# Kernel optimization log

Hardware: AMD Instinct MI355X
Metric: run time of the kernel (lower is better)

Reference implementation:

```python
import math
import jax, jax.numpy as jnp
import numpy as np

B, T, D, H = 4, 1024, 1024, 8
HD = D // H  # head_dim = 128

def _trigram_dirs():
    # 8 trigrams = all sign combinations in {−1,+1}^3, L2-normalized (p=2, dim=1)
    t = np.array([[(i >> b & 1) * 2 - 1 for b in (2, 1, 0)] for i in range(8)], dtype=np.float32)
    return jnp.asarray(t / np.linalg.norm(t, axis=1, keepdims=True))

def setup_inputs() -> dict:
    key = jax.random.key(0)
    k1, k2, k3, k4 = jax.random.split(key, 4)
    x = jax.random.normal(k1, (B, T, D), dtype=jnp.float32)
    Wqkv = jax.random.normal(k2, (D, 3 * D), dtype=jnp.float32) * 0.02
    Wout = jax.random.normal(k3, (D, D), dtype=jnp.float32) * 0.02
    # head_scales init to 0 in the module; use nonzero values so the geo-bias path is exercised
    head_scales = jax.random.normal(k4, (H,), dtype=jnp.float32) * 0.1
    head_dirs = _trigram_dirs()  # [H, 3] buffer
    return {"x": x, "Wqkv": Wqkv, "Wout": Wout, "head_scales": head_scales, "head_dirs": head_dirs}

def reference(x, Wqkv, Wout, head_scales, head_dirs):
    b, t, d = x.shape
    scale = 1.0 / math.sqrt(HD)
    qkv = (x @ Wqkv).reshape(b, t, 3, H, HD)
    qkv = jnp.transpose(qkv, (2, 0, 3, 1, 4))  # [3, B, H, T, HD]
    q, k, v = qkv[0], qkv[1], qkv[2]
    # scores: [B, H, T, T]
    scores = jnp.einsum('bhqd,bhkd->bhqk', q, k) * scale
    # rank-1 trigram geometric bias from first 3 dims of q/k
    q_proj = jnp.einsum('bhtd,hd->bht', q[..., :3], head_dirs)
    k_proj = jnp.einsum('bhtd,hd->bht', k[..., :3], head_dirs)
    geo_bias = q_proj[..., :, None] * k_proj[..., None, :]  # [B, H, T, T]
    scores = scores + head_scales[None, :, None, None] * geo_bias
    causal = jnp.tril(jnp.ones((t, t), dtype=bool))
    scores = jnp.where(causal, scores, -jnp.inf)
    attn = jax.nn.softmax(scores, axis=-1)
    out = jnp.einsum('bhqk,bhkd->bhqd', attn, v)  # [B, H, T, HD]
    out = jnp.transpose(out, (0, 2, 1, 3)).reshape(b, t, d)
    return out @ Wout
```

## Files before the change

kernel.cpp:

```cpp
#include <hip/hip_runtime.h>
#include <stdint.h>

typedef __attribute__((ext_vector_type(8))) short short8;
typedef __attribute__((ext_vector_type(4))) short short4v;
typedef __attribute__((ext_vector_type(4))) float f32x4;

__device__ __forceinline__ short f2bf(float x) {
  union { float f; uint32_t u; } c; c.f = x;
  uint32_t r = (c.u + 0x7FFFu + ((c.u >> 16) & 1u)) >> 16;
  return (short)r;
}
__device__ __forceinline__ float b2f(short s) {
  union { uint32_t u; float f; } c; c.u = ((uint32_t)(uint16_t)s) << 16;
  return c.f;
}
__device__ __forceinline__ uint32_t pack2bf(float lo, float hi) {
  return ((uint32_t)(uint16_t)f2bf(hi) << 16) | (uint32_t)(uint16_t)f2bf(lo);
}

__global__ __launch_bounds__(256) void prep_kernel(const float* __restrict__ x,
                                                   const float* __restrict__ Wqkv,
                                                   const float* __restrict__ Wout,
                                                   short* __restrict__ xb,
                                                   short* __restrict__ wqkvT,
                                                   short* __restrict__ woutT) {
  __shared__ __align__(16) short tile[32][33];
  const int bid = blockIdx.x;
  if (bid < 2048) {
    const int n4 = (4 * 1024 * 1024) / 4;
    int i = bid * 256 + threadIdx.x;
    for (; i < n4; i += 2048 * 256) {
      float4 v = reinterpret_cast<const float4*>(x)[i];
      short4v o;
      o.x = f2bf(v.x); o.y = f2bf(v.y); o.z = f2bf(v.z); o.w = f2bf(v.w);
      reinterpret_cast<short4v*>(xb)[i] = o;
    }
  } else {
    const float* in;
    short* out;
    int K, N, bx, by;
    if (bid < 2048 + 3072) {
      const int idx = bid - 2048;
      in = Wqkv; out = wqkvT; K = 1024; N = 3072; bx = idx % 96; by = idx / 96;
    } else {
      const int idx = bid - 5120;
      in = Wout; out = woutT; K = 1024; N = 1024; bx = idx % 32; by = idx / 32;
    }
    const int nb = bx * 32, kb = by * 32;
    const int tx = threadIdx.x & 31, ty = threadIdx.x >> 5;
#pragma unroll
    for (int i = 0; i < 32; i += 8)
      tile[ty + i][tx] = f2bf(in[(size_t)(kb + ty + i) * N + nb + tx]);
    __syncthreads();
#pragma unroll
    for (int i = 0; i < 32; i += 8)
      out[(size_t)(nb + ty + i) * K + kb + tx] = tile[tx][ty + i];
  }
}

__global__ __launch_bounds__(256) void vtrans_kernel(const short* __restrict__ qkvb,
                                                     short* __restrict__ vT) {
  __shared__ __align__(16) short tile[64][65];
  const int bid = blockIdx.x;
  const int b = bid / 256;
  const int kv0 = (bid % 16) * 64, c0 = ((bid / 16) % 16) * 64;
  const int tx = threadIdx.x & 15, ty = threadIdx.x >> 4;
  const short* src = qkvb + (size_t)(b * 1024) * 3072 + 2048;
#pragma unroll
  for (int i = 0; i < 64; i += 16) {
    int r = ty + i;
#pragma unroll
    for (int j = 0; j < 4; ++j)
      tile[r][tx * 4 + j] = src[(size_t)(kv0 + r) * 3072 + c0 + tx * 4 + j];
  }
  __syncthreads();
  short* dst = vT + (size_t)b * 1024 * 1024;
#pragma unroll
  for (int i = 0; i < 64; i += 16) {
    int cc = ty + i;
#pragma unroll
    for (int j = 0; j < 4; ++j)
      dst[(size_t)(c0 + cc) * 1024 + kv0 + tx * 4 + j] = tile[tx * 4 + j][cc];
  }
}

template <int OUT_BF16>
__global__ __launch_bounds__(256) void gemm_kernel(const short* __restrict__ A,
                                                   const short* __restrict__ Bt,
                                                   void* __restrict__ Cout,
                                                   int K, int ldc) {
  __shared__ __align__(16) short Al[2][128 * 32];
  __shared__ __align__(16) short Bl[2][128 * 32];
  const int t = threadIdx.x;
  const int lane = t & 63, w = t >> 6;
  const int wr = w >> 1, wc = w & 1;
  const int g = lane >> 4, c16 = lane & 15;
  const int row0 = blockIdx.y * 128, col0 = blockIdx.x * 128;

  f32x4 acc[4][4];
#pragma unroll
  for (int m = 0; m < 4; ++m)
#pragma unroll
    for (int n = 0; n < 4; ++n) {
      f32x4 z = {0.0f, 0.0f, 0.0f, 0.0f};
      acc[m][n] = z;
    }

  auto stage = [&](int buf, int kt) {
    const int k0 = kt * 32;
#pragma unroll
    for (int i = 0; i < 2; ++i) {
      const int qb = i * 256 + (t & 192);
      const int q = qb + lane;
      const int r = q >> 2;
      const int c = (q & 3) ^ ((r >> 1) & 3);
      const short* ga = A + (size_t)(row0 + r) * K + k0 + c * 8;
      const short* gb = Bt + (size_t)(col0 + r) * K + k0 + c * 8;
      __builtin_amdgcn_global_load_lds((const __attribute__((address_space(1))) void*)ga,
                                       (__attribute__((address_space(3))) void*)&Al[buf][qb * 8],
                                       16, 0, 0);
      __builtin_amdgcn_global_load_lds((const __attribute__((address_space(1))) void*)gb,
                                       (__attribute__((address_space(3))) void*)&Bl[buf][qb * 8],
                                       16, 0, 0);
    }
  };

  stage(0, 0);
  __syncthreads();
  const int NK = K >> 5;
  int cur = 0;
  const int rA0 = wr * 64 + c16;
  const int rB0 = wc * 64 + c16;
  for (int kt = 0; kt < NK; ++kt) {
    if (kt + 1 < NK) stage(cur ^ 1, kt + 1);
    short8 aF[4], bF[4];
#pragma unroll
    for (int m = 0; m < 4; ++m) {
      const int r = rA0 + m * 16;
      const int c = g ^ ((r >> 1) & 3);
      aF[m] = *reinterpret_cast<const short8*>(&Al[cur][r * 32 + c * 8]);
    }
#pragma unroll
    for (int n = 0; n < 4; ++n) {
      const int r = rB0 + n * 16;
      const int c = g ^ ((r >> 1) & 3);
      bF[n] = *reinterpret_cast<const short8*>(&Bl[cur][r * 32 + c * 8]);
    }
#pragma unroll
    for (int m = 0; m < 4; ++m)
#pragma unroll
      for (int n = 0; n < 4; ++n)
        acc[m][n] = __builtin_amdgcn_mfma_f32_16x16x32_bf16(aF[m], bF[n], acc[m][n], 0, 0, 0);
    __syncthreads();
    cur ^= 1;
  }

  const int er = row0 + wr * 64 + g * 4;
  const int ec = col0 + wc * 64 + c16;
#pragma unroll
  for (int m = 0; m < 4; ++m)
#pragma unroll
    for (int n = 0; n < 4; ++n)
#pragma unroll
      for (int j = 0; j < 4; ++j) {
        const size_t off = (size_t)(er + m * 16 + j) * ldc + ec + n * 16;
        if (OUT_BF16)
          ((short*)Cout)[off] = f2bf(acc[m][n][j]);
        else
          ((float*)Cout)[off] = acc[m][n][j];
      }
}

template <int OUT_BF16>
__global__ __launch_bounds__(256) void gemm64_kernel(const short* __restrict__ A,
                                                     const short* __restrict__ Bt,
                                                     void* __restrict__ Cout,
                                                     int K, int ldc) {
  __shared__ __align__(16) short Al[2][128 * 32];
  __shared__ __align__(16) short Bl[2][64 * 32];
  const int t = threadIdx.x;
  const int lane = t & 63, w = t >> 6;
  const int wr = w >> 1, wc = w & 1;
  const int g = lane >> 4, c16 = lane & 15;
  const int row0 = blockIdx.y * 128, col0 = blockIdx.x * 64;

  f32x4 acc[4][2];
#pragma unroll
  for (int m = 0; m < 4; ++m)
#pragma unroll
    for (int n = 0; n < 2; ++n) {
      f32x4 z = {0.0f, 0.0f, 0.0f, 0.0f};
      acc[m][n] = z;
    }

  auto stage = [&](int buf, int kt) {
    const int k0 = kt * 32;
#pragma unroll
    for (int i = 0; i < 2; ++i) {
      const int qb = i * 256 + (t & 192);
      const int q = qb + lane;
      const int r = q >> 2;
      const int c = (q & 3) ^ ((r >> 1) & 3);
      const short* ga = A + (size_t)(row0 + r) * K + k0 + c * 8;
      __builtin_amdgcn_global_load_lds((const __attribute__((address_space(1))) void*)ga,
                                       (__attribute__((address_space(3))) void*)&Al[buf][qb * 8],
                                       16, 0, 0);
    }
    {
      const int qb = (t & 192);
      const int q = qb + lane;
      const int r = q >> 2;
      const int c = (q & 3) ^ ((r >> 1) & 3);
      const short* gb = Bt + (size_t)(col0 + r) * K + k0 + c * 8;
      __builtin_amdgcn_global_load_lds((const __attribute__((address_space(1))) void*)gb,
                                       (__attribute__((address_space(3))) void*)&Bl[buf][qb * 8],
                                       16, 0, 0);
    }
  };

  stage(0, 0);
  __syncthreads();
  const int NK = K >> 5;
  int cur = 0;
  const int rA0 = wr * 64 + c16;
  const int rB0 = wc * 32 + c16;
  for (int kt = 0; kt < NK; ++kt) {
    if (kt + 1 < NK) stage(cur ^ 1, kt + 1);
    short8 aF[4], bF[2];
#pragma unroll
    for (int m = 0; m < 4; ++m) {
      const int r = rA0 + m * 16;
      const int c = g ^ ((r >> 1) & 3);
      aF[m] = *reinterpret_cast<const short8*>(&Al[cur][r * 32 + c * 8]);
    }
#pragma unroll
    for (int n = 0; n < 2; ++n) {
      const int r = rB0 + n * 16;
      const int c = g ^ ((r >> 1) & 3);
      bF[n] = *reinterpret_cast<const short8*>(&Bl[cur][r * 32 + c * 8]);
    }
#pragma unroll
    for (int m = 0; m < 4; ++m)
#pragma unroll
      for (int n = 0; n < 2; ++n)
        acc[m][n] = __builtin_amdgcn_mfma_f32_16x16x32_bf16(aF[m], bF[n], acc[m][n], 0, 0, 0);
    __syncthreads();
    cur ^= 1;
  }

  const int er = row0 + wr * 64 + g * 4;
  const int ec = col0 + wc * 32 + c16;
#pragma unroll
  for (int m = 0; m < 4; ++m)
#pragma unroll
    for (int n = 0; n < 2; ++n)
#pragma unroll
      for (int j = 0; j < 4; ++j) {
        const size_t off = (size_t)(er + m * 16 + j) * ldc + ec + n * 16;
        if (OUT_BF16)
          ((short*)Cout)[off] = f2bf(acc[m][n][j]);
        else
          ((float*)Cout)[off] = acc[m][n][j];
      }
}

__global__ __launch_bounds__(256) void attn_kernel(const short* __restrict__ qkvb,
                                                   const short* __restrict__ vT,
                                                   const float* __restrict__ head_scales,
                                                   const float* __restrict__ hdirs,
                                                   short* __restrict__ attnb) {
  __shared__ __align__(16) short Kl[2][64 * 128];
  __shared__ __align__(16) short Vl[2][128 * 64];
  __shared__ float kp_lds[2][64];

  const int bid = blockIdx.x;
  const int bh = (bid & 7) * 4 + ((bid >> 3) & 3);
  const int r2 = bid >> 5;
  const int qt = (bid < 256) ? (15 - r2) : (r2 - 8);
  const int b = bh >> 3, h = bh & 7;
  const int t = threadIdx.x, lane = t & 63, w = t >> 6;
  const int g = lane >> 4, c16 = lane & 15;
  const int q0w = qt * 64 + w * 16;
  const int q_abs = q0w + c16;

  const short* qbase = qkvb + (size_t)(b * 1024) * 3072 + h * 128;
  const short* kbase = qbase + 1024;
  const short* vtb = vT + (size_t)bh * 128 * 1024;

  const float LOG2E = 1.44269504088896f;
  const float scale2 = 0.08838834764831845f * 1.44269504088896f;
  const float d0 = hdirs[h * 3], d1 = hdirs[h * 3 + 1], d2 = hdirs[h * 3 + 2];

  short8 aQ[4];
  float hqp;
  {
    const short* qr = qbase + (size_t)(q0w + c16) * 3072;
#pragma unroll
    for (int kk = 0; kk < 4; ++kk)
      aQ[kk] = *reinterpret_cast<const short8*>(qr + kk * 32 + g * 8);
    const float hs = head_scales[h];
    hqp = hs * LOG2E * (b2f(qr[0]) * d0 + b2f(qr[1]) * d1 + b2f(qr[2]) * d2);
  }

  float m_s = -1e30f, l_s = 0.0f;
  f32x4 accO[8];
#pragma unroll
  for (int d = 0; d < 8; ++d) {
    f32x4 z = {0.0f, 0.0f, 0.0f, 0.0f};
    accO[d] = z;
  }

  auto stageKV = [&](int buf, int kvt) {
    const int kv0 = kvt * 64;
#pragma unroll
    for (int i = 0; i < 4; ++i) {
      const int s = w * 4 + i;
      {
        const int r = s * 4 + g;
        const int c = c16 ^ (r & 7);
        const short* ga = kbase + (size_t)(kv0 + r) * 3072 + c * 8;
        __builtin_amdgcn_global_load_lds((const __attribute__((address_space(1))) void*)ga,
                                         (__attribute__((address_space(3))) void*)&Kl[buf][s * 512],
                                         16, 0, 0);
      }
      {
        const int r = s * 8 + (lane >> 3);
        const int c = (lane & 7) ^ (r & 7);
        const short* ga = vtb + (size_t)r * 1024 + kv0 + c * 8;
        __builtin_amdgcn_global_load_lds((const __attribute__((address_space(1))) void*)ga,
                                         (__attribute__((address_space(3))) void*)&Vl[buf][s * 512],
                                         16, 0, 0);
      }
    }
    if (lane < 16) {
      const short* kr = kbase + (size_t)(kv0 + w * 16 + lane) * 3072;
      kp_lds[buf][w * 16 + lane] = b2f(kr[0]) * d0 + b2f(kr[1]) * d1 + b2f(kr[2]) * d2;
    }
  };

  const int nkv = qt + 1;
  stageKV(0, 0);
  __syncthreads();
  int cur = 0;
  for (int kvt = 0; kvt < nkv; ++kvt) {
    const int kv0 = kvt * 64;
    if (kvt + 1 < nkv) stageKV(cur ^ 1, kvt + 1);
    const short* Kc = Kl[cur];
    const short* Vc = Vl[cur];
    const float* kpc = kp_lds[cur];

    float p[4][4];
#pragma unroll
    for (int n = 0; n < 4; ++n) {
      f32x4 s4 = {0.0f, 0.0f, 0.0f, 0.0f};
      const int r = n * 16 + c16;
#pragma unroll
      for (int kk = 0; kk < 4; ++kk) {
        const int cch = (kk * 4 + g) ^ (r & 7);
        short8 bK = *reinterpret_cast<const short8*>(&Kc[r * 128 + cch * 8]);
        s4 = __builtin_amdgcn_mfma_f32_16x16x32_bf16(bK, aQ[kk], s4, 0, 0, 0);
      }
#pragma unroll
      for (int j = 0; j < 4; ++j) {
        const int kloc = n * 16 + g * 4 + j;
        const float v = s4[j] * scale2 + hqp * kpc[kloc];
        p[n][j] = (kv0 + kloc <= q_abs) ? v : -1e30f;
      }
    }

    float mx;
    {
      float a0 = fmaxf(fmaxf(p[0][0], p[0][1]), fmaxf(p[0][2], p[0][3]));
      float a1 = fmaxf(fmaxf(p[1][0], p[1][1]), fmaxf(p[1][2], p[1][3]));
      float a2 = fmaxf(fmaxf(p[2][0], p[2][1]), fmaxf(p[2][2], p[2][3]));
      float a3 = fmaxf(fmaxf(p[3][0], p[3][1]), fmaxf(p[3][2], p[3][3]));
      mx = fmaxf(fmaxf(a0, a1), fmaxf(a2, a3));
      mx = fmaxf(mx, __shfl_xor(mx, 16, 64));
      mx = fmaxf(mx, __shfl_xor(mx, 32, 64));
    }

    if (__any(mx - m_s > 11.54f)) {
      const float mn = fmaxf(m_s, mx);
      const float alpha = exp2f(m_s - mn);
      m_s = mn;
      l_s *= alpha;
      float aO[4];
#pragma unroll
      for (int j = 0; j < 4; ++j) aO[j] = __shfl(alpha, g * 4 + j, 64);
#pragma unroll
      for (int d = 0; d < 8; ++d)
#pragma unroll
        for (int j = 0; j < 4; ++j) accO[d][j] *= aO[j];
    }

    float s01 = 0.0f, s23 = 0.0f;
#pragma unroll
    for (int n = 0; n < 4; ++n) {
      float e0 = exp2f(p[n][0] - m_s), e1 = exp2f(p[n][1] - m_s);
      float e2 = exp2f(p[n][2] - m_s), e3 = exp2f(p[n][3] - m_s);
      p[n][0] = e0; p[n][1] = e1; p[n][2] = e2; p[n][3] = e3;
      if (n < 2) s01 += (e0 + e1) + (e2 + e3); else s23 += (e0 + e1) + (e2 + e3);
    }
    float sum = s01 + s23;
    sum += __shfl_xor(sum, 16, 64);
    sum += __shfl_xor(sum, 32, 64);
    l_s += sum;

    uint32_t pk[4][2];
#pragma unroll
    for (int n = 0; n < 4; ++n) {
      pk[n][0] = pack2bf(p[n][0], p[n][1]);
      pk[n][1] = pack2bf(p[n][2], p[n][3]);
    }

    union { uint32_t d[4]; short8 s; } aPu[2];
#pragma unroll
    for (int kk = 0; kk < 2; ++kk)
#pragma unroll
      for (int wd = 0; wd < 4; ++wd) {
        const int src = (2 * (g & 1) + (wd >> 1)) * 16 + c16;
        const uint32_t v0 = (uint32_t)__shfl((int)pk[kk * 2][wd & 1], src, 64);
        const uint32_t v1 = (uint32_t)__shfl((int)pk[kk * 2 + 1][wd & 1], src, 64);
        aPu[kk].d[wd] = (g >= 2) ? v1 : v0;
      }

#pragma unroll
    for (int dt = 0; dt < 8; ++dt) {
      const int r = dt * 16 + c16;
#pragma unroll
      for (int kk = 0; kk < 2; ++kk) {
        const int cch = (kk * 4 + g) ^ (r & 7);
        short8 bV = *reinterpret_cast<const short8*>(&Vc[r * 64 + cch * 8]);
        accO[dt] = __builtin_amdgcn_mfma_f32_16x16x32_bf16(aPu[kk].s, bV, accO[dt], 0, 0, 0);
      }
    }
    __syncthreads();
    cur ^= 1;
  }

  float linv[4];
#pragma unroll
  for (int j = 0; j < 4; ++j) linv[j] = 1.0f / __shfl(l_s, g * 4 + j, 64);
#pragma unroll
  for (int j = 0; j < 4; ++j) {
    const size_t rowoff = (size_t)(b * 1024 + q0w + g * 4 + j) * 1024 + h * 128;
#pragma unroll
    for (int dt = 0; dt < 8; ++dt)
      attnb[rowoff + dt * 16 + c16] = f2bf(accO[dt][j] * linv[j]);
  }
}

extern "C" void kernel_launch(void* const* d_in, const int* in_sizes, int n_in,
                              void* d_out, int out_size, void* d_ws, size_t ws_size,
                              hipStream_t stream) {
  const float* x = (const float*)d_in[0];
  const float* Wqkv = (const float*)d_in[1];
  const float* Wout = (const float*)d_in[2];
  const float* hscale = (const float*)d_in[3];
  const float* hdirs = (const float*)d_in[4];
  float* out = (float*)d_out;

  char* ws = (char*)d_ws;
  short* xb = (short*)(ws);
  short* wqkvT = (short*)(ws + (size_t)8 * 1024 * 1024);
  short* woutT = (short*)(ws + (size_t)14 * 1024 * 1024);
  short* qkvb = (short*)(ws + (size_t)16 * 1024 * 1024);
  short* vT = (short*)(ws + (size_t)40 * 1024 * 1024);
  short* attnb = (short*)(ws + (size_t)48 * 1024 * 1024);

  prep_kernel<<<6144, 256, 0, stream>>>(x, Wqkv, Wout, xb, wqkvT, woutT);
  gemm_kernel<1><<<dim3(24, 32), 256, 0, stream>>>(xb, wqkvT, (void*)qkvb, 1024, 3072);
  vtrans_kernel<<<1024, 256, 0, stream>>>(qkvb, vT);
  attn_kernel<<<512, 256, 0, stream>>>(qkvb, vT, hscale, hdirs, attnb);
  gemm64_kernel<0><<<dim3(16, 32), 256, 0, stream>>>(attnb, woutT, out, 1024, 1024);
}
```

Measured before the change: 110.3 us.

## Use 32x32 MFMA in attention with split-KV waves and LDS merge

Rewrites the attention kernel's inner loop to use 32x32x16 bf16 MFMAs. Each wave now handles 32 queries and half of the 64-key tile, in a 2x2 arrangement of query halves and key halves, instead of 16 queries over all keys. The two key-half partial softmax states are merged at the end through an LDS buffer that is unioned with the K/V staging memory. The fully masked diagonal sub-block is skipped for one wave, and the K swizzle widens to 16 chunks. This aims to raise MFMA efficiency and cut per-wave LDS reads of K, at the cost of an extra sync, an LDS merge pass and more accumulator registers.

Result: slower. 124.3 us (+12.7%).

```diff
diff --git a/kernel.cpp b/kernel.cpp
--- a/kernel.cpp
+++ b/kernel.cpp
@@ -4,6 +4,7 @@
 typedef __attribute__((ext_vector_type(8))) short short8;
 typedef __attribute__((ext_vector_type(4))) short short4v;
 typedef __attribute__((ext_vector_type(4))) float f32x4;
+typedef __attribute__((ext_vector_type(16))) float f32x16;
 
 __device__ __forceinline__ short f2bf(float x) {
   union { float f; uint32_t u; } c; c.f = x;
@@ -264,14 +265,23 @@
       }
 }
 
+struct AttnSmem {
+  union {
+    struct {
+      short Kl[2][64 * 128];
+      short Vl[2][128 * 64];
+      float kp[2][64];
+    } s;
+    float mg[2 * 64 * 66];
+  };
+};
+
 __global__ __launch_bounds__(256) void attn_kernel(const short* __restrict__ qkvb,
                                                    const short* __restrict__ vT,
                                                    const float* __restrict__ head_scales,
                                                    const float* __restrict__ hdirs,
                                                    short* __restrict__ attnb) {
-  __shared__ __align__(16) short Kl[2][64 * 128];
-  __shared__ __align__(16) short Vl[2][128 * 64];
-  __shared__ float kp_lds[2][64];
+  __shared__ __align__(16) AttnSmem sm;
 
   const int bid = blockIdx.x;
   const int bh = (bid & 7) * 4 + ((bid >> 3) & 3);
@@ -279,9 +289,11 @@
   const int qt = (bid < 256) ? (15 - r2) : (r2 - 8);
   const int b = bh >> 3, h = bh & 7;
   const int t = threadIdx.x, lane = t & 63, w = t >> 6;
+  const int hk = w >> 1, hq = w & 1;
   const int g = lane >> 4, c16 = lane & 15;
-  const int q0w = qt * 64 + w * 16;
-  const int q_abs = q0w + c16;
+  const int l31 = lane & 31, lh = lane >> 5;
+  const int q0w = qt * 64 + hq * 32;
+  const int q_abs = q0w + l31;
 
   const short* qbase = qkvb + (size_t)(b * 1024) * 3072 + h * 128;
   const short* kbase = qbase + 1024;
@@ -291,23 +303,23 @@
   const float scale2 = 0.08838834764831845f * 1.44269504088896f;
   const float d0 = hdirs[h * 3], d1 = hdirs[h * 3 + 1], d2 = hdirs[h * 3 + 2];
 
-  short8 aQ[4];
+  short8 aQ[8];
   float hqp;
   {
-    const short* qr = qbase + (size_t)(q0w + c16) * 3072;
-#pragma unroll
-    for (int kk = 0; kk < 4; ++kk)
-      aQ[kk] = *reinterpret_cast<const short8*>(qr + kk * 32 + g * 8);
+    const short* qr = qbase + (size_t)q_abs * 3072;
+#pragma unroll
+    for (int dd = 0; dd < 8; ++dd)
+      aQ[dd] = *reinterpret_cast<const short8*>(qr + dd * 16 + lh * 8);
     const float hs = head_scales[h];
     hqp = hs * LOG2E * (b2f(qr[0]) * d0 + b2f(qr[1]) * d1 + b2f(qr[2]) * d2);
   }
 
   float m_s = -1e30f, l_s = 0.0f;
-  f32x4 accO[8];
-#pragma unroll
-  for (int d = 0; d < 8; ++d) {
-    f32x4 z = {0.0f, 0.0f, 0.0f, 0.0f};
-    accO[d] = z;
+  f32x16 accO[4];
+#pragma unroll
+  for (int dc = 0; dc < 4; ++dc) {
+    f32x16 z = {0, 0, 0, 0, 0, 0, 0, 0, 0, 0, 0, 0, 0, 0, 0, 0};
+    accO[dc] = z;
   }
 
   auto stageKV = [&](int buf, int kvt) {
@@ -317,10 +329,10 @@
       const int s = w * 4 + i;
       {
         const int r = s * 4 + g;
-        const int c = c16 ^ (r & 7);
+        const int c = c16 ^ (r & 15);
         const short* ga = kbase + (size_t)(kv0 + r) * 3072 + c * 8;
         __builtin_amdgcn_global_load_lds((const __attribute__((address_space(1))) void*)ga,
-                                         (__attribute__((address_space(3))) void*)&Kl[buf][s * 512],
+                                         (__attribute__((address_space(3))) void*)&sm.s.Kl[buf][s * 512],
                                          16, 0, 0);
       }
       {
@@ -328,13 +340,13 @@
         const int c = (lane & 7) ^ (r & 7);
         const short* ga = vtb + (size_t)r * 1024 + kv0 + c * 8;
         __builtin_amdgcn_global_load_lds((const __attribute__((address_space(1))) void*)ga,
-                                         (__attribute__((address_space(3))) void*)&Vl[buf][s * 512],
+                                         (__attribute__((address_space(3))) void*)&sm.s.Vl[buf][s * 512],
                                          16, 0, 0);
       }
     }
     if (lane < 16) {
       const short* kr = kbase + (size_t)(kv0 + w * 16 + lane) * 3072;
-      kp_lds[buf][w * 16 + lane] = b2f(kr[0]) * d0 + b2f(kr[1]) * d1 + b2f(kr[2]) * d2;
+      sm.s.kp[buf][w * 16 + lane] = b2f(kr[0]) * d0 + b2f(kr[1]) * d1 + b2f(kr[2]) * d2;
     }
   };
 
@@ -345,108 +357,118 @@
   for (int kvt = 0; kvt < nkv; ++kvt) {
     const int kv0 = kvt * 64;
     if (kvt + 1 < nkv) stageKV(cur ^ 1, kvt + 1);
-    const short* Kc = Kl[cur];
-    const short* Vc = Vl[cur];
-    const float* kpc = kp_lds[cur];
-
-    float p[4][4];
-#pragma unroll
-    for (int n = 0; n < 4; ++n) {
-      f32x4 s4 = {0.0f, 0.0f, 0.0f, 0.0f};
-      const int r = n * 16 + c16;
-#pragma unroll
-      for (int kk = 0; kk < 4; ++kk) {
-        const int cch = (kk * 4 + g) ^ (r & 7);
-        short8 bK = *reinterpret_cast<const short8*>(&Kc[r * 128 + cch * 8]);
-        s4 = __builtin_amdgcn_mfma_f32_16x16x32_bf16(bK, aQ[kk], s4, 0, 0, 0);
-      }
-#pragma unroll
-      for (int j = 0; j < 4; ++j) {
-        const int kloc = n * 16 + g * 4 + j;
-        const float v = s4[j] * scale2 + hqp * kpc[kloc];
-        p[n][j] = (kv0 + kloc <= q_abs) ? v : -1e30f;
-      }
-    }
-
-    float mx;
-    {
-      float a0 = fmaxf(fmaxf(p[0][0], p[0][1]), fmaxf(p[0][2], p[0][3]));
-      float a1 = fmaxf(fmaxf(p[1][0], p[1][1]), fmaxf(p[1][2], p[1][3]));
-      float a2 = fmaxf(fmaxf(p[2][0], p[2][1]), fmaxf(p[2][2], p[2][3]));
-      float a3 = fmaxf(fmaxf(p[3][0], p[3][1]), fmaxf(p[3][2], p[3][3]));
-      mx = fmaxf(fmaxf(a0, a1), fmaxf(a2, a3));
-      mx = fmaxf(mx, __shfl_xor(mx, 16, 64));
-      mx = fmaxf(mx, __shfl_xor(mx, 32, 64));
-    }
-
-    if (__any(mx - m_s > 11.54f)) {
-      const float mn = fmaxf(m_s, mx);
-      const float alpha = exp2f(m_s - mn);
-      m_s = mn;
-      l_s *= alpha;
-      float aO[4];
-#pragma unroll
-      for (int j = 0; j < 4; ++j) aO[j] = __shfl(alpha, g * 4 + j, 64);
-#pragma unroll
-      for (int d = 0; d < 8; ++d)
-#pragma unroll
-        for (int j = 0; j < 4; ++j) accO[d][j] *= aO[j];
-    }
-
-    float s01 = 0.0f, s23 = 0.0f;
-#pragma unroll
-    for (int n = 0; n < 4; ++n) {
-      float e0 = exp2f(p[n][0] - m_s), e1 = exp2f(p[n][1] - m_s);
-      float e2 = exp2f(p[n][2] - m_s), e3 = exp2f(p[n][3] - m_s);
-      p[n][0] = e0; p[n][1] = e1; p[n][2] = e2; p[n][3] = e3;
-      if (n < 2) s01 += (e0 + e1) + (e2 + e3); else s23 += (e0 + e1) + (e2 + e3);
-    }
-    float sum = s01 + s23;
-    sum += __shfl_xor(sum, 16, 64);
-    sum += __shfl_xor(sum, 32, 64);
-    l_s += sum;
-
-    uint32_t pk[4][2];
-#pragma unroll
-    for (int n = 0; n < 4; ++n) {
-      pk[n][0] = pack2bf(p[n][0], p[n][1]);
-      pk[n][1] = pack2bf(p[n][2], p[n][3]);
-    }
-
-    union { uint32_t d[4]; short8 s; } aPu[2];
-#pragma unroll
-    for (int kk = 0; kk < 2; ++kk)
-#pragma unroll
-      for (int wd = 0; wd < 4; ++wd) {
-        const int src = (2 * (g & 1) + (wd >> 1)) * 16 + c16;
-        const uint32_t v0 = (uint32_t)__shfl((int)pk[kk * 2][wd & 1], src, 64);
-        const uint32_t v1 = (uint32_t)__shfl((int)pk[kk * 2 + 1][wd & 1], src, 64);
-        aPu[kk].d[wd] = (g >= 2) ? v1 : v0;
-      }
-
-#pragma unroll
-    for (int dt = 0; dt < 8; ++dt) {
-      const int r = dt * 16 + c16;
-#pragma unroll
-      for (int kk = 0; kk < 2; ++kk) {
-        const int cch = (kk * 4 + g) ^ (r & 7);
-        short8 bV = *reinterpret_cast<const short8*>(&Vc[r * 64 + cch * 8]);
-        accO[dt] = __builtin_amdgcn_mfma_f32_16x16x32_bf16(aPu[kk].s, bV, accO[dt], 0, 0, 0);
+    const short* Kc = sm.s.Kl[cur];
+    const short* Vc = sm.s.Vl[cur];
+    const float* kpc = sm.s.kp[cur];
+    const bool active = !(kvt == qt && hk == 1 && hq == 0);
+
+    if (active) {
+      f32x16 s4 = {0, 0, 0, 0, 0, 0, 0, 0, 0, 0, 0, 0, 0, 0, 0, 0};
+      const int kr = hk * 32 + l31;
+      const int rx = kr & 15;
+#pragma unroll
+      for (int dd = 0; dd < 8; ++dd) {
+        short8 aK = *reinterpret_cast<const short8*>(&Kc[kr * 128 + (((dd << 1) | lh) ^ rx) * 8]);
+        s4 = __builtin_amdgcn_mfma_f32_32x32x16_bf16(aK, aQ[dd], s4, 0, 0, 0);
+      }
+      float p[16];
+#pragma unroll
+      for (int reg = 0; reg < 16; ++reg) {
+        const int row = (reg & 3) + 8 * (reg >> 2) + 4 * lh;
+        const int kva = kv0 + hk * 32 + row;
+        const float v = s4[reg] * scale2 + hqp * kpc[hk * 32 + row];
+        p[reg] = (kva <= q_abs) ? v : -1e30f;
+      }
+      float mx;
+      {
+        float a0 = fmaxf(fmaxf(p[0], p[1]), fmaxf(p[2], p[3]));
+        float a1 = fmaxf(fmaxf(p[4], p[5]), fmaxf(p[6], p[7]));
+        float a2 = fmaxf(fmaxf(p[8], p[9]), fmaxf(p[10], p[11]));
+        float a3 = fmaxf(fmaxf(p[12], p[13]), fmaxf(p[14], p[15]));
+        mx = fmaxf(fmaxf(a0, a1), fmaxf(a2, a3));
+        mx = fmaxf(mx, __shfl_xor(mx, 32, 64));
+      }
+      if (__any(mx - m_s > 11.54f)) {
+        const float mn = fmaxf(m_s, mx);
+        const float alpha = exp2f(m_s - mn);
+        m_s = mn;
+        l_s *= alpha;
+        float aR[16];
+#pragma unroll
+        for (int reg = 0; reg < 16; ++reg)
+          aR[reg] = __shfl(alpha, (reg & 3) + 8 * (reg >> 2) + 4 * lh, 64);
+#pragma unroll
+        for (int dc = 0; dc < 4; ++dc)
+#pragma unroll
+          for (int reg = 0; reg < 16; ++reg) accO[dc][reg] *= aR[reg];
+      }
+      float sum = 0.0f;
+#pragma unroll
+      for (int reg = 0; reg < 16; ++reg) {
+        p[reg] = exp2f(p[reg] - m_s);
+        sum += p[reg];
+      }
+      sum += __shfl_xor(sum, 32, 64);
+      l_s += sum;
+      uint32_t pk[8], sw[8];
+#pragma unroll
+      for (int i = 0; i < 8; ++i) pk[i] = pack2bf(p[2 * i], p[2 * i + 1]);
+#pragma unroll
+      for (int i = 0; i < 8; ++i) sw[i] = (uint32_t)__shfl_xor((int)pk[i], 32, 64);
+      union { uint32_t d[4]; short8 s; } A1, A2;
+      A1.d[0] = lh ? sw[2] : pk[0];
+      A1.d[1] = lh ? sw[3] : pk[1];
+      A1.d[2] = lh ? pk[2] : sw[0];
+      A1.d[3] = lh ? pk[3] : sw[1];
+      A2.d[0] = lh ? sw[6] : pk[4];
+      A2.d[1] = lh ? sw[7] : pk[5];
+      A2.d[2] = lh ? pk[6] : sw[4];
+      A2.d[3] = lh ? pk[7] : sw[5];
+#pragma unroll
+      for (int dc = 0; dc < 4; ++dc) {
+        const int vr = dc * 32 + l31;
+        const int vx = vr & 7;
+        short8 bV0 = *reinterpret_cast<const short8*>(&Vc[vr * 64 + (((hk << 2) | lh) ^ vx) * 8]);
+        short8 bV1 = *reinterpret_cast<const short8*>(&Vc[vr * 64 + (((hk << 2) | 2 | lh) ^ vx) * 8]);
+        accO[dc] = __builtin_amdgcn_mfma_f32_32x32x16_bf16(A1.s, bV0, accO[dc], 0, 0, 0);
+        accO[dc] = __builtin_amdgcn_mfma_f32_32x32x16_bf16(A2.s, bV1, accO[dc], 0, 0, 0);
       }
     }
     __syncthreads();
     cur ^= 1;
   }
 
-  float linv[4];
-#pragma unroll
-  for (int j = 0; j < 4; ++j) linv[j] = 1.0f / __shfl(l_s, g * 4 + j, 64);
-#pragma unroll
-  for (int j = 0; j < 4; ++j) {
-    const size_t rowoff = (size_t)(b * 1024 + q0w + g * 4 + j) * 1024 + h * 128;
-#pragma unroll
-    for (int dt = 0; dt < 8; ++dt)
-      attnb[rowoff + dt * 16 + c16] = f2bf(accO[dt][j] * linv[j]);
+  const int base = (hq * 64 + lane) * 66;
+  if (hk == 1) {
+    sm.mg[base] = m_s;
+    sm.mg[base + 1] = l_s;
+#pragma unroll
+    for (int dc = 0; dc < 4; ++dc)
+#pragma unroll
+      for (int reg = 0; reg < 16; ++reg) sm.mg[base + 2 + dc * 16 + reg] = accO[dc][reg];
+  }
+  __syncthreads();
+  if (hk == 0) {
+    const float m1 = sm.mg[base], l1 = sm.mg[base + 1];
+    const float mn = fmaxf(m_s, m1);
+    const float a0 = exp2f(m_s - mn), a1 = exp2f(m1 - mn);
+    const float linv = 1.0f / (l_s * a0 + l1 * a1);
+    const float f0 = a0 * linv, f1 = a1 * linv;
+    float fR0[16], fR1[16];
+#pragma unroll
+    for (int reg = 0; reg < 16; ++reg) {
+      const int row = (reg & 3) + 8 * (reg >> 2) + 4 * lh;
+      fR0[reg] = __shfl(f0, row, 64);
+      fR1[reg] = __shfl(f1, row, 64);
+    }
+#pragma unroll
+    for (int dc = 0; dc < 4; ++dc)
+#pragma unroll
+      for (int reg = 0; reg < 16; ++reg) {
+        const int row = (reg & 3) + 8 * (reg >> 2) + 4 * lh;
+        const float o = accO[dc][reg] * fR0[reg] + sm.mg[base + 2 + dc * 16 + reg] * fR1[reg];
+        attnb[(size_t)(b * 1024 + q0w + row) * 1024 + h * 128 + dc * 32 + l31] = f2bf(o);
+      }
   }
 }
 
```
